# Optimization experiments

Hardware: AMD Instinct MI355X
Metric: run time of the kernel (lower is better)

## Reference

```python
import jax, jax.numpy as jnp
import numpy as np

N, D, N_SIGMAS = 4096, 128, 75

def _pairwise_sq_dist(x):
    # squared euclidean distances, [N, N]
    sq = jnp.sum(x * x, axis=1)
    d2 = sq[:, None] + sq[None, :] - 2.0 * (x @ x.T)
    return jnp.maximum(d2, 0.0)

def setup_inputs() -> dict:
    key = jax.random.key(0)
    kx, ky = jax.random.split(key)
    x = jax.random.normal(kx, (N, D), dtype=jnp.float32)
    # realistic label kernel: RBF over random 10-dim label embeddings
    y = jax.random.normal(ky, (N, 10), dtype=jnp.float32)
    label_kernel = jnp.exp(-_pairwise_sq_dist(y))
    return {"x": x, "label_kernel": label_kernel}

def reference(x, label_kernel):
    n = x.shape[0]
    d2 = _pairwise_sq_dist(x)              # [N, N] squared distances
    nz = d2 > 0
    # safe sqrt (avoid nan grads on diagonal zeros)
    dist = jnp.where(nz, jnp.sqrt(jnp.where(nz, d2, 1.0)), 0.0)
    # mean of nonzero distances (distance[distance != 0].mean())
    mean_distance = jnp.sum(dist) / jnp.sum(nz).astype(x.dtype)
    lo = 0.1 * mean_distance
    hi = 10.0 * mean_distance
    step = (hi - lo) / N_SIGMAS
    sigmas = lo + step * jnp.arange(N_SIGMAS, dtype=x.dtype)  # np.arange equivalent

    label_norm = jnp.linalg.norm(label_kernel)

    def alignment_loss(sigma):
        K = jnp.exp(-d2 / (sigma * sigma))
        return jnp.sum(K * label_kernel) / (jnp.linalg.norm(K) * label_norm)

    losses = jax.lax.map(alignment_loss, sigmas)   # sequential sigma sweep
    sigma_opt = sigmas[jnp.argmax(losses)]         # first max, like np.argwhere(...).item()

    A = jnp.exp(-d2 / (sigma_opt * sigma_opt)) / n
    return A
```

## Files before the change

### kernel.cpp

```cpp
#include <hip/hip_runtime.h>
#include <hip/hip_bf16.h>

#define NN 4096
#define DD 128
#define NS 75
#define TOT (NN * NN)

#define BT 128
#define NBD2 (NN / BT)
#define GRID_D2 (NBD2 * (NBD2 + 1) / 2)

#define SB 64
#define NBSW (NN / SB)
#define NTILES (NBSW * (NBSW + 1) / 2)
#define GRID_SW (NTILES / 2)

typedef float v2f __attribute__((ext_vector_type(2)));
typedef float f32x4 __attribute__((ext_vector_type(4)));
typedef short bf16x8 __attribute__((ext_vector_type(8)));

__device__ __forceinline__ float fexp2(float v) { return __builtin_amdgcn_exp2f(v); }

__device__ __forceinline__ void gload_lds16(const void* g, void* l) {
    __builtin_amdgcn_global_load_lds(
        (const __attribute__((address_space(1))) unsigned int*)g,
        (__attribute__((address_space(3))) unsigned int*)l,
        16, 0, 0);
}

template <int CTRL>
__device__ __forceinline__ float dpp_add(float x) {
    int y = __builtin_amdgcn_update_dpp(0, __float_as_int(x), CTRL, 0xf, 0xf, true);
    return x + __int_as_float(y);
}
__device__ __forceinline__ float wave_sum(float x) {
    x = dpp_add<0x111>(x);
    x = dpp_add<0x112>(x);
    x = dpp_add<0x114>(x);
    x = dpp_add<0x118>(x);
    x = dpp_add<0x142>(x);
    x = dpp_add<0x143>(x);
    return x;
}

__device__ __forceinline__ void tri_decode(int t, int nb, int& bi, int& bj) {
    int b = 0, rem = t;
    while (rem >= nb - b) { rem -= nb - b; ++b; }
    bi = b; bj = b + rem;
}

__device__ __forceinline__ void cvt_split(const float4& v0, const float4& v1,
                                          bf16x8& hi, bf16x8& lo) {
    float f[8] = {v0.x, v0.y, v0.z, v0.w, v1.x, v1.y, v1.z, v1.w};
#pragma unroll
    for (int j = 0; j < 8; ++j) {
        unsigned b = __float_as_uint(f[j]);
        hi[j] = (short)(b >> 16);
        float l = f[j] - __uint_as_float(b & 0xFFFF0000u);
        lo[j] = (short)(__float_as_uint(l) >> 16);
    }
}

__device__ __forceinline__ int coarse_window(const double* KL, const double* KK) {
    double best = -1.0;
    int bk = 0;
    for (int k = 0; k < 25; ++k) {
        double loss = KL[k] / sqrt(KK[k]);
        if (loss > best) { best = loss; bk = k; }
    }
    int wv = 3 * bk - 2;
    if (wv < 0) wv = 0;
    if (wv > NS - 5) wv = NS - 5;
    return wv;
}

#define WS_DSUM 0
#define WS_NZC  8
#define WS_KL   16
#define WS_KK   (16 + 256)
#define WS_SQ   (16 + 512)
#define WS_CSIG (WS_SQ + 4 * NN)

__global__ void k_rowsq(const float* __restrict__ x, float* __restrict__ sq,
                        double* __restrict__ dsum, unsigned long long* __restrict__ nzc) {
    int tid = blockIdx.x * blockDim.x + threadIdx.x;
    if (tid == 0) { *dsum = 0.0; *nzc = 0ull; }
    if (tid < NN) {
        const float4* row = (const float4*)(x + (size_t)tid * DD);
        float s = 0.f;
#pragma unroll
        for (int i = 0; i < DD / 4; ++i) {
            float4 v = row[i];
            s += v.x * v.x + v.y * v.y + v.z * v.z + v.w * v.w;
        }
        sq[tid] = s;
    }
}

__launch_bounds__(256)
__global__ void k_d2(const float* __restrict__ x, const float* __restrict__ sq,
                     float* __restrict__ d2, double* __restrict__ dsum,
                     unsigned long long* __restrict__ nzc) {
    __shared__ float st[4][32][68];
    __shared__ double red_d[4];
    __shared__ int red_n[4];

    int bi, bj;
    tri_decode(blockIdx.x, NBD2, bi, bj);
    const int r0 = bi * BT, c0 = bj * BT;
    const int tid = threadIdx.x;
    const int l  = tid & 63, wid = tid >> 6;
    const int wr = wid >> 1, wc = wid & 1;
    const int lr = l & 15;
    const int lk = (l >> 4) * 8;
    const int l4 = (l >> 4) * 4;

    const int ar = r0 + wr * 64 + lr;
    const int br = c0 + wc * 64 + lr;

    f32x4 acc[4][4];
#pragma unroll
    for (int a = 0; a < 4; ++a)
#pragma unroll
        for (int b = 0; b < 4; ++b) acc[a][b] = (f32x4){0.f, 0.f, 0.f, 0.f};

#pragma unroll 1
    for (int kc = 0; kc < 4; ++kc) {
        const int k0 = kc * 32 + lk;
        bf16x8 ah[4], al[4], bh[4], bl[4];
#pragma unroll
        for (int t = 0; t < 4; ++t) {
            const float* pa = x + (size_t)(ar + t * 16) * DD + k0;
            float4 a0 = *(const float4*)pa;
            float4 a1 = *(const float4*)(pa + 4);
            cvt_split(a0, a1, ah[t], al[t]);
            const float* pb = x + (size_t)(br + t * 16) * DD + k0;
            float4 b0 = *(const float4*)pb;
            float4 b1 = *(const float4*)(pb + 4);
            cvt_split(b0, b1, bh[t], bl[t]);
        }
#pragma unroll
        for (int a = 0; a < 4; ++a)
#pragma unroll
            for (int b = 0; b < 4; ++b) {
                acc[a][b] = __builtin_amdgcn_mfma_f32_16x16x32_bf16(ah[a], bh[b], acc[a][b], 0, 0, 0);
                acc[a][b] = __builtin_amdgcn_mfma_f32_16x16x32_bf16(ah[a], bl[b], acc[a][b], 0, 0, 0);
                acc[a][b] = __builtin_amdgcn_mfma_f32_16x16x32_bf16(al[a], bh[b], acc[a][b], 0, 0, 0);
            }
    }

    float myd = 0.f;
    int myn = 0;
#pragma unroll
    for (int a = 0; a < 4; ++a) {
        const int grb = r0 + wr * 64 + a * 16 + l4;
        float4 sqr = *(const float4*)(sq + grb);
        float sr[4] = {sqr.x, sqr.y, sqr.z, sqr.w};
#pragma unroll
        for (int b = 0; b < 4; ++b) {
            const float sc = sq[c0 + wc * 64 + b * 16 + lr];
#pragma unroll
            for (int v = 0; v < 4; ++v) {
                float d = fmaxf(sr[v] + sc - 2.f * acc[a][b][v], 0.f);
                acc[a][b][v] = d;
                if (d > 0.f) { myd += sqrtf(d); ++myn; }
            }
        }
    }

    const int row0 = r0 + wr * 64, col0 = c0 + wc * 64;
#pragma unroll
    for (int p = 0; p < 2; ++p) {
#pragma unroll
        for (int ha = 0; ha < 2; ++ha) {
            const int a = 2 * p + ha;
#pragma unroll
            for (int b = 0; b < 4; ++b)
#pragma unroll
                for (int v = 0; v < 4; ++v)
                    st[wid][ha * 16 + l4 + v][b * 16 + lr] = acc[a][b][v];
        }
#pragma unroll
        for (int q = 0; q < 8; ++q) {
            const int lr2 = q * 4 + (l >> 4);
            f32x4 vv = *(const f32x4*)&st[wid][lr2][(l & 15) * 4];
            *(f32x4*)(d2 + (size_t)(row0 + p * 32 + lr2) * NN + col0 + (l & 15) * 4) = vv;
        }
        if (bi != bj) {
#pragma unroll
            for (int q = 0; q < 8; ++q) {
                const int tc = q * 8 + (l >> 3);
                const int trb = (l & 7) * 4;
                f32x4 vv = {st[wid][trb + 0][tc], st[wid][trb + 1][tc],
                            st[wid][trb + 2][tc], st[wid][trb + 3][tc]};
                *(f32x4*)(d2 + (size_t)(col0 + tc) * NN + row0 + p * 32 + trb) = vv;
            }
        }
    }

    const int w = (bi == bj) ? 1 : 2;
    float sd = wave_sum(myd);
    float sn = wave_sum((float)myn);
    if ((tid & 63) == 63) { red_d[wid] = (double)sd; red_n[wid] = (int)sn; }
    __syncthreads();
    if (tid == 0) {
        double td = red_d[0] + red_d[1] + red_d[2] + red_d[3];
        int tn = red_n[0] + red_n[1] + red_n[2] + red_n[3];
        atomicAdd(dsum, td * (double)w);
        atomicAdd(nzc, (unsigned long long)(tn * w));
    }
}

__global__ void k_sigmas(const double* __restrict__ dsum, const unsigned long long* __restrict__ nzc,
                         float* __restrict__ csig, double* __restrict__ KL, double* __restrict__ KK) {
    int t = threadIdx.x;
    float mean = (float)(*dsum / (double)(*nzc));
    float lo = 0.1f * mean;
    float hi = 10.0f * mean;
    float step = (hi - lo) / (float)NS;
    if (t < NS) {
        float s = lo + step * (float)t;
        csig[t] = (float)(1.4426950408889634 / ((double)s * (double)s));
    }
    if (t < 32) { KL[t] = 0.0; KK[t] = 0.0; }
}

template <bool ADD, int CH, int S0, int STRIDE, int NSLOT>
__device__ __forceinline__ void sweep_phase(const v2f* nd, const v2f* ll,
                                            const float* __restrict__ csig, int off,
                                            double part[4][2 * NSLOT],
                                            int wave, int lane, float w) {
    float c[CH];
#pragma unroll
    for (int s = 0; s < CH; ++s)
        c[s] = __int_as_float(__builtin_amdgcn_readfirstlane(
                   __float_as_int(csig[off + STRIDE * (S0 + s)])));
    v2f akl[CH], akk[CH];
#pragma unroll
    for (int s = 0; s < CH; ++s) { akl[s] = (v2f){0.f, 0.f}; akk[s] = (v2f){0.f, 0.f}; }

#pragma unroll
    for (int e = 0; e < 8; ++e) {
        v2f ndv = nd[e], L = ll[e];
#pragma unroll
        for (int s = 0; s < CH; ++s) {
            v2f arg = ndv * c[s];
            v2f K = {fexp2(arg.x), fexp2(arg.y)};
            akl[s] = __builtin_elementwise_fma(K, L, akl[s]);
            akk[s] = __builtin_elementwise_fma(K, K, akk[s]);
        }
    }

#pragma unroll
    for (int s = 0; s < CH; ++s) {
        float v1 = wave_sum(akl[s].x + akl[s].y);
        float v2 = wave_sum(akk[s].x + akk[s].y);
        if (lane == 63) {
            if (ADD) {
                part[wave][S0 + s]         += (double)(v1 * w);
                part[wave][NSLOT + S0 + s] += (double)(v2 * w);
            } else {
                part[wave][S0 + s]         = (double)(v1 * w);
                part[wave][NSLOT + S0 + s] = (double)(v2 * w);
            }
        }
    }
}

__device__ __forceinline__ void sweep_load_direct(const float* __restrict__ d2,
                                                  const float* __restrict__ lk,
                                                  int r0, int c0, v2f* nd, v2f* ll) {
    const int rr = threadIdx.x >> 4;
    const int c4 = (threadIdx.x & 15) * 4;
#pragma unroll
    for (int it = 0; it < 4; ++it) {
        size_t off = (size_t)(r0 + rr + 16 * it) * NN + c0 + c4;
        float4 dv = *(const float4*)(d2 + off);
        float4 lv = *(const float4*)(lk + off);
        nd[it * 2 + 0] = (v2f){-dv.x, -dv.y};
        nd[it * 2 + 1] = (v2f){-dv.z, -dv.w};
        ll[it * 2 + 0] = (v2f){lv.x, lv.y};
        ll[it * 2 + 1] = (v2f){lv.z, lv.w};
    }
}

__device__ __forceinline__ void sweep_prefetch(const float* __restrict__ d2,
                                               const float* __restrict__ lk,
                                               int r0, int c0, char* wbuf) {
    const int l = threadIdx.x & 63;
    const int wave4 = (threadIdx.x >> 6) * 4;
    const int rr = wave4 + (l >> 4);
    const int c4 = (l & 15) * 4;
#pragma unroll
    for (int q = 0; q < 4; ++q) {
        size_t off = (size_t)(r0 + rr + 16 * q) * NN + c0 + c4;
        gload_lds16(d2 + off, wbuf + q * 1024);
        gload_lds16(lk + off, wbuf + (4 + q) * 1024);
    }
}

__device__ __forceinline__ void sweep_unpack(const char* wbuf, v2f* nd, v2f* ll) {
    const int l = threadIdx.x & 63;
#pragma unroll
    for (int q = 0; q < 4; ++q) {
        f32x4 dv = *(const f32x4*)(wbuf + q * 1024 + l * 16);
        f32x4 lv = *(const f32x4*)(wbuf + (4 + q) * 1024 + l * 16);
        nd[q * 2 + 0] = (v2f){-dv[0], -dv[1]};
        nd[q * 2 + 1] = (v2f){-dv[2], -dv[3]};
        ll[q * 2 + 0] = (v2f){lv[0], lv[1]};
        ll[q * 2 + 1] = (v2f){lv[2], lv[3]};
    }
}

__launch_bounds__(256, 3)
__global__ void k_sweep_coarse(const float* __restrict__ d2, const float* __restrict__ lk,
                               const float* __restrict__ csig, double* __restrict__ KL,
                               double* __restrict__ KK) {
    __shared__ char pbuf[4][8192];
    __shared__ double part[4][50];
    const int lane = threadIdx.x & 63, wave = threadIdx.x >> 6;

    int t0 = blockIdx.x * 2, t1 = t0 + 1;
    int bi0, bj0, bi1, bj1;
    tri_decode(t0, NBSW, bi0, bj0);
    tri_decode(t1, NBSW, bi1, bj1);
    const float w0 = (bi0 == bj0) ? 1.f : 2.f;
    const float w1 = (bi1 == bj1) ? 1.f : 2.f;

    sweep_prefetch(d2, lk, bi1 * SB, bj1 * SB, &pbuf[wave][0]);
    v2f nd[8], ll[8];
    sweep_load_direct(d2, lk, bi0 * SB, bj0 * SB, nd, ll);

    sweep_phase<false, 13, 0, 3, 25>(nd, ll, csig, 0, part, wave, lane, w0);
    sweep_phase<false, 12, 13, 3, 25>(nd, ll, csig, 0, part, wave, lane, w0);

    asm volatile("s_waitcnt vmcnt(0)" ::: "memory");
    sweep_unpack(&pbuf[wave][0], nd, ll);

    sweep_phase<true, 13, 0, 3, 25>(nd, ll, csig, 0, part, wave, lane, w1);
    sweep_phase<true, 12, 13, 3, 25>(nd, ll, csig, 0, part, wave, lane, w1);

    __syncthreads();
    const int t = threadIdx.x;
    if (t < 50) {
        double v = part[0][t] + part[1][t] + part[2][t] + part[3][t];
        if (t < 25) atomicAdd(&KL[t], v);
        else        atomicAdd(&KK[t - 25], v);
    }
}

__launch_bounds__(256, 3)
__global__ void k_sweep_refine(const float* __restrict__ d2, const float* __restrict__ lk,
                               const float* __restrict__ csig, double* __restrict__ KL,
                               double* __restrict__ KK) {
    __shared__ char pbuf[4][8192];
    __shared__ double part[4][10];
    __shared__ int w0_sh;
    if (threadIdx.x == 0) w0_sh = coarse_window(KL, KK);
    const int lane = threadIdx.x & 63, wave = threadIdx.x >> 6;

    int t0 = blockIdx.x * 2, t1 = t0 + 1;
    int bi0, bj0, bi1, bj1;
    tri_decode(t0, NBSW, bi0, bj0);
    tri_decode(t1, NBSW, bi1, bj1);
    const float wt0 = (bi0 == bj0) ? 1.f : 2.f;
    const float wt1 = (bi1 == bj1) ? 1.f : 2.f;

    sweep_prefetch(d2, lk, bi1 * SB, bj1 * SB, &pbuf[wave][0]);
    v2f nd[8], ll[8];
    sweep_load_direct(d2, lk, bi0 * SB, bj0 * SB, nd, ll);
    __syncthreads();
    const int s0 = w0_sh;

    sweep_phase<false, 5, 0, 1, 5>(nd, ll, csig, s0, part, wave, lane, wt0);

    asm volatile("s_waitcnt vmcnt(0)" ::: "memory");
    sweep_unpack(&pbuf[wave][0], nd, ll);

    sweep_phase<true, 5, 0, 1, 5>(nd, ll, csig, s0, part, wave, lane, wt1);

    __syncthreads();
    const int t = threadIdx.x;
    if (t < 10) {
        double v = part[0][t] + part[1][t] + part[2][t] + part[3][t];
        if (t < 5) atomicAdd(&KL[25 + t], v);
        else       atomicAdd(&KK[25 + t - 5], v);
    }
}

__launch_bounds__(256)
__global__ void k_final(float* __restrict__ d2, const double* __restrict__ KL,
                        const double* __restrict__ KK, const float* __restrict__ csig) {
    __shared__ float cc_sh;
    if (threadIdx.x == 0) {
        int wv = coarse_window(KL, KK);
        double best = -1.0;
        int bk = 0;
        for (int k = 0; k < 5; ++k) {
            double loss = KL[25 + k] / sqrt(KK[25 + k]);
            if (loss > best) { best = loss; bk = k; }
        }
        cc_sh = csig[wv + bk];
    }
    __syncthreads();
    const float cc = cc_sh;
    const float inv_n = 1.0f / (float)NN;
    const int nthreads = gridDim.x * blockDim.x;
    float4* p = (float4*)d2;
    for (int i = blockIdx.x * blockDim.x + threadIdx.x; i < TOT / 4; i += nthreads) {
        float4 v = p[i];
        v.x = fexp2(-v.x * cc) * inv_n;
        v.y = fexp2(-v.y * cc) * inv_n;
        v.z = fexp2(-v.z * cc) * inv_n;
        v.w = fexp2(-v.w * cc) * inv_n;
        p[i] = v;
    }
}

extern "C" void kernel_launch(void* const* d_in, const int* in_sizes, int n_in,
                              void* d_out, int out_size, void* d_ws, size_t ws_size,
                              hipStream_t stream) {
    const float* x  = (const float*)d_in[0];
    const float* lk = (const float*)d_in[1];
    float* out = (float*)d_out;
    char* ws = (char*)d_ws;

    double* dsum = (double*)(ws + WS_DSUM);
    unsigned long long* nzc = (unsigned long long*)(ws + WS_NZC);
    double* KL = (double*)(ws + WS_KL);
    double* KK = (double*)(ws + WS_KK);
    float* sqv  = (float*)(ws + WS_SQ);
    float* csig = (float*)(ws + WS_CSIG);

    hipLaunchKernelGGL(k_rowsq, dim3(NN / 256), dim3(256), 0, stream, x, sqv, dsum, nzc);
    hipLaunchKernelGGL(k_d2, dim3(GRID_D2), dim3(256), 0, stream, x, sqv, out, dsum, nzc);
    hipLaunchKernelGGL(k_sigmas, dim3(1), dim3(128), 0, stream, dsum, nzc, csig, KL, KK);
    hipLaunchKernelGGL(k_sweep_coarse, dim3(GRID_SW), dim3(256), 0, stream, out, lk, csig, KL, KK);
    hipLaunchKernelGGL(k_sweep_refine, dim3(GRID_SW), dim3(256), 0, stream, out, lk, csig, KL, KK);
    hipLaunchKernelGGL(k_final, dim3(2048), dim3(256), 0, stream, out, KL, KK, csig);
}
```

Baseline: 147.7 us.

## Store only upper-triangle d2 tiles and mirror during final exp pass

k_d2 now computes 64x64 upper-triangular tiles and writes only the upper-triangle tile, skipping the transposed store. k_final walks the same triangular tiles, applies the exp scaling, and writes both the tile and its transpose from shared memory. This removes the transposed d2 write in the distance stage and moves the mirroring to the final pass. The sweep kernels must read only upper-triangle tiles for correctness, and the smaller 64x64 tile in k_d2 reduces reuse of x across blocks.

```diff
diff --git a/kernel.cpp b/kernel.cpp
--- a/kernel.cpp
+++ b/kernel.cpp
@@ -5,10 +5,6 @@
 #define DD 128
 #define NS 75
 #define TOT (NN * NN)
-
-#define BT 128
-#define NBD2 (NN / BT)
-#define GRID_D2 (NBD2 * (NBD2 + 1) / 2)
 
 #define SB 64
 #define NBSW (NN / SB)
@@ -61,6 +57,56 @@
     }
 }
 
+__device__ __forceinline__ void d2_tile(const float* __restrict__ x,
+                                        const float* __restrict__ sq,
+                                        int tr, int tc, float dv[4][4]) {
+    const int l = threadIdx.x & 63, wid = threadIdx.x >> 6;
+    const int lr = l & 15;
+    const int lkb = (l >> 4) * 8;
+    const int arow = tr * 64 + wid * 16 + lr;
+
+    f32x4 acc[4];
+#pragma unroll
+    for (int ct = 0; ct < 4; ++ct) acc[ct] = (f32x4){0.f, 0.f, 0.f, 0.f};
+
+#pragma unroll 1
+    for (int kc = 0; kc < 4; ++kc) {
+        const int k0 = kc * 32 + lkb;
+        bf16x8 ah, al;
+        {
+            const float* pa = x + (size_t)arow * DD + k0;
+            float4 a0 = *(const float4*)pa;
+            float4 a1 = *(const float4*)(pa + 4);
+            cvt_split(a0, a1, ah, al);
+        }
+        bf16x8 bh[4], bl[4];
+#pragma unroll
+        for (int ct = 0; ct < 4; ++ct) {
+            const float* pb = x + (size_t)(tc * 64 + ct * 16 + lr) * DD + k0;
+            float4 b0 = *(const float4*)pb;
+            float4 b1 = *(const float4*)(pb + 4);
+            cvt_split(b0, b1, bh[ct], bl[ct]);
+        }
+#pragma unroll
+        for (int ct = 0; ct < 4; ++ct) {
+            acc[ct] = __builtin_amdgcn_mfma_f32_16x16x32_bf16(ah, bh[ct], acc[ct], 0, 0, 0);
+            acc[ct] = __builtin_amdgcn_mfma_f32_16x16x32_bf16(ah, bl[ct], acc[ct], 0, 0, 0);
+            acc[ct] = __builtin_amdgcn_mfma_f32_16x16x32_bf16(al, bh[ct], acc[ct], 0, 0, 0);
+        }
+    }
+
+    const int rb = tr * 64 + wid * 16 + (l >> 4) * 4;
+    float4 s4 = *(const float4*)(sq + rb);
+    float sr[4] = {s4.x, s4.y, s4.z, s4.w};
+#pragma unroll
+    for (int ct = 0; ct < 4; ++ct) {
+        float sc = sq[tc * 64 + ct * 16 + lr];
+#pragma unroll
+        for (int v = 0; v < 4; ++v)
+            dv[ct][v] = fmaxf(sr[v] + sc - 2.f * acc[ct][v], 0.f);
+    }
+}
+
 __device__ __forceinline__ int coarse_window(const double* KL, const double* KK) {
     double best = -1.0;
     int bk = 0;
@@ -97,112 +143,52 @@
     }
 }
 
-__launch_bounds__(256)
 __global__ void k_d2(const float* __restrict__ x, const float* __restrict__ sq,
                      float* __restrict__ d2, double* __restrict__ dsum,
                      unsigned long long* __restrict__ nzc) {
-    __shared__ float st[4][32][68];
+    __shared__ float st[64][68];
     __shared__ double red_d[4];
     __shared__ int red_n[4];
 
-    int bi, bj;
-    tri_decode(blockIdx.x, NBD2, bi, bj);
-    const int r0 = bi * BT, c0 = bj * BT;
+    int ti, tj;
+    tri_decode(blockIdx.x, NBSW, ti, tj);
+    const int r0 = ti * SB, c0 = tj * SB;
     const int tid = threadIdx.x;
-    const int l  = tid & 63, wid = tid >> 6;
-    const int wr = wid >> 1, wc = wid & 1;
+    const int l = tid & 63, wid = tid >> 6;
     const int lr = l & 15;
-    const int lk = (l >> 4) * 8;
-    const int l4 = (l >> 4) * 4;
-
-    const int ar = r0 + wr * 64 + lr;
-    const int br = c0 + wc * 64 + lr;
-
-    f32x4 acc[4][4];
-#pragma unroll
-    for (int a = 0; a < 4; ++a)
-#pragma unroll
-        for (int b = 0; b < 4; ++b) acc[a][b] = (f32x4){0.f, 0.f, 0.f, 0.f};
-
-#pragma unroll 1
-    for (int kc = 0; kc < 4; ++kc) {
-        const int k0 = kc * 32 + lk;
-        bf16x8 ah[4], al[4], bh[4], bl[4];
-#pragma unroll
-        for (int t = 0; t < 4; ++t) {
-            const float* pa = x + (size_t)(ar + t * 16) * DD + k0;
-            float4 a0 = *(const float4*)pa;
-            float4 a1 = *(const float4*)(pa + 4);
-            cvt_split(a0, a1, ah[t], al[t]);
-            const float* pb = x + (size_t)(br + t * 16) * DD + k0;
-            float4 b0 = *(const float4*)pb;
-            float4 b1 = *(const float4*)(pb + 4);
-            cvt_split(b0, b1, bh[t], bl[t]);
-        }
-#pragma unroll
-        for (int a = 0; a < 4; ++a)
-#pragma unroll
-            for (int b = 0; b < 4; ++b) {
-                acc[a][b] = __builtin_amdgcn_mfma_f32_16x16x32_bf16(ah[a], bh[b], acc[a][b], 0, 0, 0);
-                acc[a][b] = __builtin_amdgcn_mfma_f32_16x16x32_bf16(ah[a], bl[b], acc[a][b], 0, 0, 0);
-                acc[a][b] = __builtin_amdgcn_mfma_f32_16x16x32_bf16(al[a], bh[b], acc[a][b], 0, 0, 0);
-            }
-    }
+
+    float dv[4][4];
+    d2_tile(x, sq, ti, tj, dv);
 
     float myd = 0.f;
     int myn = 0;
 #pragma unroll
-    for (int a = 0; a < 4; ++a) {
-        const int grb = r0 + wr * 64 + a * 16 + l4;
-        float4 sqr = *(const float4*)(sq + grb);
-        float sr[4] = {sqr.x, sqr.y, sqr.z, sqr.w};
-#pragma unroll
-        for (int b = 0; b < 4; ++b) {
-            const float sc = sq[c0 + wc * 64 + b * 16 + lr];
-#pragma unroll
-            for (int v = 0; v < 4; ++v) {
-                float d = fmaxf(sr[v] + sc - 2.f * acc[a][b][v], 0.f);
-                acc[a][b][v] = d;
-                if (d > 0.f) { myd += sqrtf(d); ++myn; }
-            }
-        }
-    }
-
-    const int row0 = r0 + wr * 64, col0 = c0 + wc * 64;
-#pragma unroll
-    for (int p = 0; p < 2; ++p) {
-#pragma unroll
-        for (int ha = 0; ha < 2; ++ha) {
-            const int a = 2 * p + ha;
-#pragma unroll
-            for (int b = 0; b < 4; ++b)
-#pragma unroll
-                for (int v = 0; v < 4; ++v)
-                    st[wid][ha * 16 + l4 + v][b * 16 + lr] = acc[a][b][v];
-        }
-#pragma unroll
-        for (int q = 0; q < 8; ++q) {
-            const int lr2 = q * 4 + (l >> 4);
-            f32x4 vv = *(const f32x4*)&st[wid][lr2][(l & 15) * 4];
-            *(f32x4*)(d2 + (size_t)(row0 + p * 32 + lr2) * NN + col0 + (l & 15) * 4) = vv;
-        }
-        if (bi != bj) {
-#pragma unroll
-            for (int q = 0; q < 8; ++q) {
-                const int tc = q * 8 + (l >> 3);
-                const int trb = (l & 7) * 4;
-                f32x4 vv = {st[wid][trb + 0][tc], st[wid][trb + 1][tc],
-                            st[wid][trb + 2][tc], st[wid][trb + 3][tc]};
-                *(f32x4*)(d2 + (size_t)(col0 + tc) * NN + row0 + p * 32 + trb) = vv;
-            }
-        }
-    }
-
-    const int w = (bi == bj) ? 1 : 2;
+    for (int ct = 0; ct < 4; ++ct)
+#pragma unroll
+        for (int v = 0; v < 4; ++v) {
+            float d = dv[ct][v];
+            if (d > 0.f) { myd += sqrtf(d); ++myn; }
+        }
+    const int w = (ti == tj) ? 1 : 2;
     float sd = wave_sum(myd);
     float sn = wave_sum((float)myn);
-    if ((tid & 63) == 63) { red_d[wid] = (double)sd; red_n[wid] = (int)sn; }
+    if (l == 63) { red_d[wid] = (double)sd; red_n[wid] = (int)sn; }
+
+    const int lrow = wid * 16 + (l >> 4) * 4;
+#pragma unroll
+    for (int ct = 0; ct < 4; ++ct)
+#pragma unroll
+        for (int v = 0; v < 4; ++v)
+            st[lrow + v][ct * 16 + lr] = dv[ct][v];
     __syncthreads();
+
+#pragma unroll
+    for (int q = 0; q < 4; ++q) {
+        const int rr = q * 16 + (tid >> 4);
+        const int cc = (tid & 15) * 4;
+        *(f32x4*)(d2 + (size_t)(r0 + rr) * NN + c0 + cc) = *(const f32x4*)&st[rr][cc];
+    }
+
     if (tid == 0) {
         double td = red_d[0] + red_d[1] + red_d[2] + red_d[3];
         int tn = red_n[0] + red_n[1] + red_n[2] + red_n[3];
@@ -388,9 +374,9 @@
     }
 }
 
-__launch_bounds__(256)
 __global__ void k_final(float* __restrict__ d2, const double* __restrict__ KL,
                         const double* __restrict__ KK, const float* __restrict__ csig) {
+    __shared__ float st[64][68];
     __shared__ float cc_sh;
     if (threadIdx.x == 0) {
         int wv = coarse_window(KL, KK);
@@ -405,15 +391,35 @@
     __syncthreads();
     const float cc = cc_sh;
     const float inv_n = 1.0f / (float)NN;
-    const int nthreads = gridDim.x * blockDim.x;
-    float4* p = (float4*)d2;
-    for (int i = blockIdx.x * blockDim.x + threadIdx.x; i < TOT / 4; i += nthreads) {
-        float4 v = p[i];
-        v.x = fexp2(-v.x * cc) * inv_n;
-        v.y = fexp2(-v.y * cc) * inv_n;
-        v.z = fexp2(-v.z * cc) * inv_n;
-        v.w = fexp2(-v.w * cc) * inv_n;
-        p[i] = v;
+
+    int ti, tj;
+    tri_decode(blockIdx.x, NBSW, ti, tj);
+    const int r0 = ti * SB, c0 = tj * SB;
+    const int tid = threadIdx.x;
+
+#pragma unroll
+    for (int q = 0; q < 4; ++q) {
+        const int rr = q * 16 + (tid >> 4);
+        const int cc4 = (tid & 15) * 4;
+        float* p = d2 + (size_t)(r0 + rr) * NN + c0 + cc4;
+        f32x4 v = *(const f32x4*)p;
+        v[0] = fexp2(-v[0] * cc) * inv_n;
+        v[1] = fexp2(-v[1] * cc) * inv_n;
+        v[2] = fexp2(-v[2] * cc) * inv_n;
+        v[3] = fexp2(-v[3] * cc) * inv_n;
+        *(f32x4*)p = v;
+        *(f32x4*)&st[rr][cc4] = v;
+    }
+
+    if (ti != tj) {
+        __syncthreads();
+#pragma unroll
+        for (int q = 0; q < 4; ++q) {
+            const int tc = q * 16 + (tid >> 4);
+            const int rb = (tid & 15) * 4;
+            f32x4 vv = {st[rb + 0][tc], st[rb + 1][tc], st[rb + 2][tc], st[rb + 3][tc]};
+            *(f32x4*)(d2 + (size_t)(c0 + tc) * NN + r0 + rb) = vv;
+        }
     }
 }
 
@@ -433,9 +439,9 @@
     float* csig = (float*)(ws + WS_CSIG);
 
     hipLaunchKernelGGL(k_rowsq, dim3(NN / 256), dim3(256), 0, stream, x, sqv, dsum, nzc);
-    hipLaunchKernelGGL(k_d2, dim3(GRID_D2), dim3(256), 0, stream, x, sqv, out, dsum, nzc);
+    hipLaunchKernelGGL(k_d2, dim3(NTILES), dim3(256), 0, stream, x, sqv, out, dsum, nzc);
     hipLaunchKernelGGL(k_sigmas, dim3(1), dim3(128), 0, stream, dsum, nzc, csig, KL, KK);
     hipLaunchKernelGGL(k_sweep_coarse, dim3(GRID_SW), dim3(256), 0, stream, out, lk, csig, KL, KK);
     hipLaunchKernelGGL(k_sweep_refine, dim3(GRID_SW), dim3(256), 0, stream, out, lk, csig, KL, KK);
-    hipLaunchKernelGGL(k_final, dim3(2048), dim3(256), 0, stream, out, KL, KK, csig);
-}
+    hipLaunchKernelGGL(k_final, dim3(NTILES), dim3(256), 0, stream, out, KL, KK, csig);
+}
```

Result: slower. 175.2 us (+18.7%).

## Write only upper-triangle d2 tiles and mirror symmetric output in final exp pass

Applied to the files above, without the earlier changes.

k_d2 now writes only the upper-triangle block tiles, using 512 threads per block with a shared 64x128 staging buffer, and no longer does the transposed mirror write. k_final now runs one block per upper-triangle 64x64 tile: it reads that tile, applies the exp, and writes both the tile and its transpose. This cuts the d2 write traffic roughly in half and removes the full-matrix read in the final pass. The catch is that the sweep kernels must touch only the upper triangle, and the final kernel does strided transposed writes.

```diff
diff --git a/kernel.cpp b/kernel.cpp
--- a/kernel.cpp
+++ b/kernel.cpp
@@ -97,50 +97,53 @@
     }
 }
 
-__launch_bounds__(256)
+__launch_bounds__(512, 2)
 __global__ void k_d2(const float* __restrict__ x, const float* __restrict__ sq,
                      float* __restrict__ d2, double* __restrict__ dsum,
                      unsigned long long* __restrict__ nzc) {
-    __shared__ float st[4][32][68];
-    __shared__ double red_d[4];
-    __shared__ int red_n[4];
+    __shared__ float st[64][132];
+    __shared__ double red_d[8];
+    __shared__ int red_n[8];
 
     int bi, bj;
     tri_decode(blockIdx.x, NBD2, bi, bj);
     const int r0 = bi * BT, c0 = bj * BT;
     const int tid = threadIdx.x;
-    const int l  = tid & 63, wid = tid >> 6;
+    const int l = tid & 63, wid = tid >> 6;
     const int wr = wid >> 1, wc = wid & 1;
     const int lr = l & 15;
     const int lk = (l >> 4) * 8;
     const int l4 = (l >> 4) * 4;
 
-    const int ar = r0 + wr * 64 + lr;
-    const int br = c0 + wc * 64 + lr;
-
-    f32x4 acc[4][4];
-#pragma unroll
-    for (int a = 0; a < 4; ++a)
+    const int arow = r0 + wr * 32 + lr;
+    const int brow = c0 + wc * 64 + lr;
+
+    f32x4 acc[2][4];
+#pragma unroll
+    for (int a = 0; a < 2; ++a)
 #pragma unroll
         for (int b = 0; b < 4; ++b) acc[a][b] = (f32x4){0.f, 0.f, 0.f, 0.f};
 
 #pragma unroll 1
     for (int kc = 0; kc < 4; ++kc) {
         const int k0 = kc * 32 + lk;
-        bf16x8 ah[4], al[4], bh[4], bl[4];
-#pragma unroll
-        for (int t = 0; t < 4; ++t) {
-            const float* pa = x + (size_t)(ar + t * 16) * DD + k0;
+        bf16x8 ah[2], al[2], bh[4], bl[4];
+#pragma unroll
+        for (int a = 0; a < 2; ++a) {
+            const float* pa = x + (size_t)(arow + a * 16) * DD + k0;
             float4 a0 = *(const float4*)pa;
             float4 a1 = *(const float4*)(pa + 4);
-            cvt_split(a0, a1, ah[t], al[t]);
-            const float* pb = x + (size_t)(br + t * 16) * DD + k0;
+            cvt_split(a0, a1, ah[a], al[a]);
+        }
+#pragma unroll
+        for (int b = 0; b < 4; ++b) {
+            const float* pb = x + (size_t)(brow + b * 16) * DD + k0;
             float4 b0 = *(const float4*)pb;
             float4 b1 = *(const float4*)(pb + 4);
-            cvt_split(b0, b1, bh[t], bl[t]);
-        }
-#pragma unroll
-        for (int a = 0; a < 4; ++a)
+            cvt_split(b0, b1, bh[b], bl[b]);
+        }
+#pragma unroll
+        for (int a = 0; a < 2; ++a)
 #pragma unroll
             for (int b = 0; b < 4; ++b) {
                 acc[a][b] = __builtin_amdgcn_mfma_f32_16x16x32_bf16(ah[a], bh[b], acc[a][b], 0, 0, 0);
@@ -152,8 +155,8 @@
     float myd = 0.f;
     int myn = 0;
 #pragma unroll
-    for (int a = 0; a < 4; ++a) {
-        const int grb = r0 + wr * 64 + a * 16 + l4;
+    for (int a = 0; a < 2; ++a) {
+        const int grb = r0 + wr * 32 + a * 16 + l4;
         float4 sqr = *(const float4*)(sq + grb);
         float sr[4] = {sqr.x, sqr.y, sqr.z, sqr.w};
 #pragma unroll
@@ -167,45 +170,39 @@
             }
         }
     }
-
-    const int row0 = r0 + wr * 64, col0 = c0 + wc * 64;
-#pragma unroll
-    for (int p = 0; p < 2; ++p) {
-#pragma unroll
-        for (int ha = 0; ha < 2; ++ha) {
-            const int a = 2 * p + ha;
-#pragma unroll
-            for (int b = 0; b < 4; ++b)
-#pragma unroll
-                for (int v = 0; v < 4; ++v)
-                    st[wid][ha * 16 + l4 + v][b * 16 + lr] = acc[a][b][v];
-        }
-#pragma unroll
-        for (int q = 0; q < 8; ++q) {
-            const int lr2 = q * 4 + (l >> 4);
-            f32x4 vv = *(const f32x4*)&st[wid][lr2][(l & 15) * 4];
-            *(f32x4*)(d2 + (size_t)(row0 + p * 32 + lr2) * NN + col0 + (l & 15) * 4) = vv;
-        }
-        if (bi != bj) {
-#pragma unroll
-            for (int q = 0; q < 8; ++q) {
-                const int tc = q * 8 + (l >> 3);
-                const int trb = (l & 7) * 4;
-                f32x4 vv = {st[wid][trb + 0][tc], st[wid][trb + 1][tc],
-                            st[wid][trb + 2][tc], st[wid][trb + 3][tc]};
-                *(f32x4*)(d2 + (size_t)(col0 + tc) * NN + row0 + p * 32 + trb) = vv;
-            }
-        }
-    }
-
     const int w = (bi == bj) ? 1 : 2;
     float sd = wave_sum(myd);
     float sn = wave_sum((float)myn);
-    if ((tid & 63) == 63) { red_d[wid] = (double)sd; red_n[wid] = (int)sn; }
-    __syncthreads();
+    if (l == 63) { red_d[wid] = (double)sd; red_n[wid] = (int)sn; }
+
+#pragma unroll
+    for (int p = 0; p < 2; ++p) {
+        __syncthreads();
+        if ((wr >> 1) == p) {
+            const int lrow = (wr & 1) * 32 + l4;
+#pragma unroll
+            for (int a = 0; a < 2; ++a)
+#pragma unroll
+                for (int b = 0; b < 4; ++b)
+#pragma unroll
+                    for (int v = 0; v < 4; ++v)
+                        st[lrow + (a == 1 ? 16 : 0) + v][wc * 64 + b * 16 + lr] = acc[a][b][v];
+        }
+        __syncthreads();
+#pragma unroll
+        for (int q = 0; q < 4; ++q) {
+            const int rr = q * 16 + (tid >> 5);
+            const int cc = (tid & 31) * 4;
+            *(f32x4*)(d2 + (size_t)(r0 + p * 64 + rr) * NN + c0 + cc) =
+                *(const f32x4*)&st[rr][cc];
+        }
+    }
+
     if (tid == 0) {
-        double td = red_d[0] + red_d[1] + red_d[2] + red_d[3];
-        int tn = red_n[0] + red_n[1] + red_n[2] + red_n[3];
+        double td = 0.0;
+        int tn = 0;
+#pragma unroll
+        for (int q = 0; q < 8; ++q) { td += red_d[q]; tn += red_n[q]; }
         atomicAdd(dsum, td * (double)w);
         atomicAdd(nzc, (unsigned long long)(tn * w));
     }
@@ -388,9 +385,9 @@
     }
 }
 
-__launch_bounds__(256)
 __global__ void k_final(float* __restrict__ d2, const double* __restrict__ KL,
                         const double* __restrict__ KK, const float* __restrict__ csig) {
+    __shared__ float st[64][68];
     __shared__ float cc_sh;
     if (threadIdx.x == 0) {
         int wv = coarse_window(KL, KK);
@@ -405,15 +402,35 @@
     __syncthreads();
     const float cc = cc_sh;
     const float inv_n = 1.0f / (float)NN;
-    const int nthreads = gridDim.x * blockDim.x;
-    float4* p = (float4*)d2;
-    for (int i = blockIdx.x * blockDim.x + threadIdx.x; i < TOT / 4; i += nthreads) {
-        float4 v = p[i];
-        v.x = fexp2(-v.x * cc) * inv_n;
-        v.y = fexp2(-v.y * cc) * inv_n;
-        v.z = fexp2(-v.z * cc) * inv_n;
-        v.w = fexp2(-v.w * cc) * inv_n;
-        p[i] = v;
+
+    int ti, tj;
+    tri_decode(blockIdx.x, NBSW, ti, tj);
+    const int r0 = ti * SB, c0 = tj * SB;
+    const int tid = threadIdx.x;
+
+#pragma unroll
+    for (int q = 0; q < 4; ++q) {
+        const int rr = q * 16 + (tid >> 4);
+        const int cc4 = (tid & 15) * 4;
+        float* p = d2 + (size_t)(r0 + rr) * NN + c0 + cc4;
+        f32x4 v = *(const f32x4*)p;
+        v[0] = fexp2(-v[0] * cc) * inv_n;
+        v[1] = fexp2(-v[1] * cc) * inv_n;
+        v[2] = fexp2(-v[2] * cc) * inv_n;
+        v[3] = fexp2(-v[3] * cc) * inv_n;
+        *(f32x4*)p = v;
+        *(f32x4*)&st[rr][cc4] = v;
+    }
+
+    if (ti != tj) {
+        __syncthreads();
+#pragma unroll
+        for (int q = 0; q < 4; ++q) {
+            const int tc = q * 16 + (tid >> 4);
+            const int rb = (tid & 15) * 4;
+            f32x4 vv = {st[rb + 0][tc], st[rb + 1][tc], st[rb + 2][tc], st[rb + 3][tc]};
+            *(f32x4*)(d2 + (size_t)(c0 + tc) * NN + r0 + rb) = vv;
+        }
     }
 }
 
@@ -433,9 +450,9 @@
     float* csig = (float*)(ws + WS_CSIG);
 
     hipLaunchKernelGGL(k_rowsq, dim3(NN / 256), dim3(256), 0, stream, x, sqv, dsum, nzc);
-    hipLaunchKernelGGL(k_d2, dim3(GRID_D2), dim3(256), 0, stream, x, sqv, out, dsum, nzc);
+    hipLaunchKernelGGL(k_d2, dim3(GRID_D2), dim3(512), 0, stream, x, sqv, out, dsum, nzc);
     hipLaunchKernelGGL(k_sigmas, dim3(1), dim3(128), 0, stream, dsum, nzc, csig, KL, KK);
     hipLaunchKernelGGL(k_sweep_coarse, dim3(GRID_SW), dim3(256), 0, stream, out, lk, csig, KL, KK);
     hipLaunchKernelGGL(k_sweep_refine, dim3(GRID_SW), dim3(256), 0, stream, out, lk, csig, KL, KK);
-    hipLaunchKernelGGL(k_final, dim3(2048), dim3(256), 0, stream, out, KL, KK, csig);
-}
+    hipLaunchKernelGGL(k_final, dim3(NTILES), dim3(256), 0, stream, out, KL, KK, csig);
+}
```

After: 150.4 us. No clear change (+1.8%).
